# Kernel tuning notes

Measured on AMD Instinct MI355X. Metric: run time of the kernel, lower is better.

The kernel has to match this reference:

```python
import jax, jax.numpy as jnp
import numpy as np

E = 800000   # num edges
C = 64       # in_channels == out_channels
H = 4        # heads
D = C // H   # head_dim
N = 50000    # num_nodes


def setup_inputs() -> dict:
    key = jax.random.key(0)
    ks = jax.random.split(key, 10)
    s = 1.0 / np.sqrt(C)
    inp = {
        "query": jax.random.normal(ks[0], (E, C), jnp.float32),
        "key": jax.random.normal(ks[1], (E, C), jnp.float32),
        "value": jax.random.normal(ks[2], (E, C), jnp.float32),
        "Wq": jax.random.normal(ks[3], (C, C), jnp.float32) * s,
        "bq": jax.random.normal(ks[4], (C,), jnp.float32) * s,
        "Wk": jax.random.normal(ks[5], (C, C), jnp.float32) * s,
        "bk": jax.random.normal(ks[6], (C,), jnp.float32) * s,
        "Wv": jax.random.normal(ks[7], (C, C), jnp.float32) * s,
        "bv": jax.random.normal(ks[8], (C,), jnp.float32) * s,
        "index": jnp.sort(jax.random.randint(ks[9], (E,), 0, N, jnp.int32)),
        "num_nodes": N,
    }
    return inp


def reference(query, key, value, Wq, bq, Wk, bk, Wv, bv, index, num_nodes):
    # per-edge linear projections (groups=1 Linear)
    q = (query @ Wq + bq).reshape(E, H, D)
    k = (key @ Wk + bk).reshape(E, H, D)
    v = (value @ Wv + bv).reshape(E, H, D)

    # per-edge per-head scalar attention score
    score = jnp.einsum("ehd,ehd->eh", q, k) / jnp.sqrt(jnp.float32(D))  # [E, H]

    # restricted softmax over edges grouped by destination node (margin=0)
    smax = jax.ops.segment_max(score, index, num_segments=num_nodes)  # [N, H]
    smax = jnp.maximum(smax, 0.0)  # clamp(min=0); also fixes -inf on empty segments
    ex = jnp.exp(score - smax[index])                                  # [E, H]
    denom = jax.ops.segment_sum(ex, index, num_segments=num_nodes)    # [N, H]
    denom = denom + jnp.exp(-smax)                                     # margin - src_max with margin=0
    attn = ex / denom[index]                                           # [E, H]

    # weighted values (score is 1x1 per edge/head so this is a scale)
    out = attn[:, :, None] * v                                         # [E, H, D]
    return out.reshape(E, C)
```

## Files before the change

### kernel.cpp

```cpp
#include <hip/hip_runtime.h>
#include <hip/hip_bf16.h>
#include <math.h>

#define E_N 800000
#define C_N 64
#define H_N 4
#define D_N 16
#define NODES 50000

typedef __bf16 bf16x8 __attribute__((ext_vector_type(8)));
typedef float f32x4 __attribute__((ext_vector_type(4)));

__device__ __forceinline__ unsigned short f2bf_rne(float f) {
    unsigned int u = __float_as_uint(f);
    u += 0x7fffu + ((u >> 16) & 1u);
    return (unsigned short)(u >> 16);
}

union BfPack { bf16x8 v; unsigned short s[8]; };

__device__ __forceinline__ bf16x8 load_row_bf16(const float* __restrict__ p) {
    const float4* p4 = (const float4*)p;
    float4 a = p4[0], b = p4[1];
    BfPack u;
    u.s[0] = f2bf_rne(a.x); u.s[1] = f2bf_rne(a.y);
    u.s[2] = f2bf_rne(a.z); u.s[3] = f2bf_rne(a.w);
    u.s[4] = f2bf_rne(b.x); u.s[5] = f2bf_rne(b.y);
    u.s[6] = f2bf_rne(b.z); u.s[7] = f2bf_rne(b.w);
    return u.v;
}

__global__ void wt_kernel(const float* __restrict__ Wq,
                          const float* __restrict__ Wk,
                          const float* __restrict__ Wv,
                          unsigned short* __restrict__ wt) {
    int t = threadIdx.x;
    for (int w = 0; w < 3; ++w) {
        const float* W = (w == 0) ? Wq : (w == 1) ? Wk : Wv;
        for (int i = t; i < 4096; i += 256) {
            int o = i >> 6, c = i & 63;
            wt[w * 4096 + i] = f2bf_rne(W[c * 64 + o]);
        }
    }
}

__global__ __launch_bounds__(256) void score_kernel(
    const float* __restrict__ query, const float* __restrict__ key,
    const float* __restrict__ bq, const float* __restrict__ bk,
    const int* __restrict__ index,
    const unsigned short* __restrict__ wt,
    float* __restrict__ score, int* __restrict__ smax) {
    int lane = threadIdx.x & 63;
    int wid  = threadIdx.x >> 6;
    int e0   = blockIdx.x * 64 + wid * 16;
    int m    = lane & 15, quad = lane >> 4;

    const float* qrow = query + (size_t)(e0 + m) * 64 + quad * 8;
    const float* krow = key   + (size_t)(e0 + m) * 64 + quad * 8;
    bf16x8 aq0 = load_row_bf16(qrow);
    bf16x8 aq1 = load_row_bf16(qrow + 32);
    bf16x8 ak0 = load_row_bf16(krow);
    bf16x8 ak1 = load_row_bf16(krow + 32);

    const bf16x8* wq8 = (const bf16x8*)(wt);
    const bf16x8* wk8 = (const bf16x8*)(wt + 4096);

    for (int h = 0; h < H_N; ++h) {
        int bi0 = (h * 16 + m) * 8 + quad;
        int bi1 = bi0 + 4;
        f32x4 cq = {0.f, 0.f, 0.f, 0.f}, ck = {0.f, 0.f, 0.f, 0.f};
        cq = __builtin_amdgcn_mfma_f32_16x16x32_bf16(aq0, wq8[bi0], cq, 0, 0, 0);
        cq = __builtin_amdgcn_mfma_f32_16x16x32_bf16(aq1, wq8[bi1], cq, 0, 0, 0);
        ck = __builtin_amdgcn_mfma_f32_16x16x32_bf16(ak0, wk8[bi0], ck, 0, 0, 0);
        ck = __builtin_amdgcn_mfma_f32_16x16x32_bf16(ak1, wk8[bi1], ck, 0, 0, 0);
        float bqv = bq[h * 16 + m], bkv = bk[h * 16 + m];
        float p[4];
        #pragma unroll
        for (int r = 0; r < 4; ++r) p[r] = (cq[r] + bqv) * (ck[r] + bkv);
        #pragma unroll
        for (int r = 0; r < 4; ++r) {
            p[r] += __shfl_xor(p[r], 1, 64);
            p[r] += __shfl_xor(p[r], 2, 64);
            p[r] += __shfl_xor(p[r], 4, 64);
            p[r] += __shfl_xor(p[r], 8, 64);
        }
        if (m == 0) {
            #pragma unroll
            for (int r = 0; r < 4; ++r) {
                int e = e0 + quad * 4 + r;
                float s = p[r] * 0.25f;
                score[e * 4 + h] = s;
                if (s > 0.f) {
                    int n = index[e];
                    atomicMax(smax + n * 4 + h, __float_as_int(s));
                }
            }
        }
    }
}

__global__ void denom_init_kernel(const int* __restrict__ smax,
                                  float* __restrict__ denom) {
    int i = blockIdx.x * 256 + threadIdx.x;
    if (i < NODES * H_N) denom[i] = __expf(-__int_as_float(smax[i]));
}

__global__ __launch_bounds__(256) void expsum_kernel(
    const float* __restrict__ score, const int* __restrict__ index,
    const int* __restrict__ smax, float* __restrict__ denom) {
    int t = blockIdx.x * 256 + threadIdx.x;
    int e = t >> 2, h = t & 3;
    int n = index[e];
    float sm = __int_as_float(smax[n * 4 + h]);
    float ex = __expf(score[t] - sm);
    atomicAdd(denom + n * 4 + h, ex);
}

__global__ __launch_bounds__(256) void out_kernel(
    const float* __restrict__ value, const float* __restrict__ bv,
    const int* __restrict__ index, const unsigned short* __restrict__ wt,
    const float* __restrict__ score, const int* __restrict__ smax_i,
    const float* __restrict__ denom, float* __restrict__ out) {
    int lane = threadIdx.x & 63;
    int wid  = threadIdx.x >> 6;
    int e0   = blockIdx.x * 64 + wid * 16;
    int m    = lane & 15, quad = lane >> 4;

    int ee = e0 + (lane >> 2), hh = lane & 3;
    int n  = index[ee];
    float sm = __int_as_float(smax_i[n * 4 + hh]);
    float attn = __expf(score[ee * 4 + hh] - sm) / denom[n * 4 + hh];

    const float* vrow = value + (size_t)(e0 + m) * 64 + quad * 8;
    bf16x8 av0 = load_row_bf16(vrow);
    bf16x8 av1 = load_row_bf16(vrow + 32);
    const bf16x8* wv8 = (const bf16x8*)(wt + 8192);

    for (int h = 0; h < H_N; ++h) {
        int bi0 = (h * 16 + m) * 8 + quad;
        f32x4 cv = {0.f, 0.f, 0.f, 0.f};
        cv = __builtin_amdgcn_mfma_f32_16x16x32_bf16(av0, wv8[bi0], cv, 0, 0, 0);
        cv = __builtin_amdgcn_mfma_f32_16x16x32_bf16(av1, wv8[bi0 + 4], cv, 0, 0, 0);
        float bvv = bv[h * 16 + m];
        #pragma unroll
        for (int r = 0; r < 4; ++r) {
            int row = quad * 4 + r;
            float a = __shfl(attn, (row << 2) | h, 64);
            out[(size_t)(e0 + row) * 64 + h * 16 + m] = (cv[r] + bvv) * a;
        }
    }
}

extern "C" void kernel_launch(void* const* d_in, const int* in_sizes, int n_in,
                              void* d_out, int out_size, void* d_ws, size_t ws_size,
                              hipStream_t stream) {
    const float* query = (const float*)d_in[0];
    const float* key   = (const float*)d_in[1];
    const float* value = (const float*)d_in[2];
    const float* Wq    = (const float*)d_in[3];
    const float* bq    = (const float*)d_in[4];
    const float* Wk    = (const float*)d_in[5];
    const float* bk    = (const float*)d_in[6];
    const float* Wv    = (const float*)d_in[7];
    const float* bv    = (const float*)d_in[8];
    const int*   index = (const int*)d_in[9];

    char* ws = (char*)d_ws;
    unsigned short* wt = (unsigned short*)ws;
    float* score = (float*)(ws + 32768);
    int*   smax  = (int*)(ws + 32768 + (size_t)E_N * 16);
    float* denom = (float*)(ws + 32768 + (size_t)E_N * 16 + (size_t)NODES * 16);

    hipMemsetAsync(smax, 0, (size_t)NODES * 16, stream);
    wt_kernel<<<1, 256, 0, stream>>>(Wq, Wk, Wv, wt);
    score_kernel<<<E_N / 64, 256, 0, stream>>>(query, key, bq, bk, index, wt,
                                               score, smax);
    denom_init_kernel<<<(NODES * H_N + 255) / 256, 256, 0, stream>>>(smax, denom);
    expsum_kernel<<<(E_N * H_N) / 256, 256, 0, stream>>>(score, index, smax, denom);
    out_kernel<<<E_N / 64, 256, 0, stream>>>(value, bv, index, wt, score, smax,
                                             denom, (float*)d_out);
}
```

Measured before the change: 740.5 us.

## Pre-reduce segment max/sum within warps before atomics and precompute reciprocal denominators

Score and expsum kernels now do a segmented shuffle scan over the 16 edges per wave (using the sorted index) so only segment-tail lanes issue atomicMax/atomicAdd, cutting atomic traffic by the average in-wave run length. A finalize kernel folds the exp(-smax) term into the denominator and stores (smax, 1/denom) pairs, so out_kernel does one float2 load and a multiply instead of two loads and a divide. Score stores become coalesced one-per-lane rather than masked writes from m==0 lanes. It adds an extra index load per lane and one more small kernel launch.

```diff
diff --git a/kernel.cpp b/kernel.cpp
--- a/kernel.cpp
+++ b/kernel.cpp
@@ -65,6 +65,12 @@
     const bf16x8* wq8 = (const bf16x8*)(wt);
     const bf16x8* wk8 = (const bf16x8*)(wt + 4096);
 
+    int erel = lane >> 2;
+    int hl   = lane & 3;
+    int rw   = erel & 3;
+    float s_mine = 0.f;
+
+    #pragma unroll
     for (int h = 0; h < H_N; ++h) {
         int bi0 = (h * 16 + m) * 8 + quad;
         int bi1 = bi0 + 4;
@@ -84,58 +90,80 @@
             p[r] += __shfl_xor(p[r], 4, 64);
             p[r] += __shfl_xor(p[r], 8, 64);
         }
-        if (m == 0) {
-            #pragma unroll
-            for (int r = 0; r < 4; ++r) {
-                int e = e0 + quad * 4 + r;
-                float s = p[r] * 0.25f;
-                score[e * 4 + h] = s;
-                if (s > 0.f) {
-                    int n = index[e];
-                    atomicMax(smax + n * 4 + h, __float_as_int(s));
-                }
-            }
-        }
-    }
-}
-
-__global__ void denom_init_kernel(const int* __restrict__ smax,
-                                  float* __restrict__ denom) {
-    int i = blockIdx.x * 256 + threadIdx.x;
-    if (i < NODES * H_N) denom[i] = __expf(-__int_as_float(smax[i]));
+        float pw = (rw == 0) ? p[0] : (rw == 1) ? p[1] : (rw == 2) ? p[2] : p[3];
+        if (h == hl) s_mine = pw * 0.25f;
+    }
+
+    score[(size_t)e0 * 4 + lane] = s_mine;
+
+    int e = e0 + erel;
+    int n = index[e];
+    float s = s_mine;
+    #pragma unroll
+    for (int d = 4; d <= 32; d <<= 1) {
+        float up = __shfl_up(s, d, 64);
+        int  nup = __shfl_up(n, d, 64);
+        if (lane >= d && nup == n) s = fmaxf(s, up);
+    }
+    bool tail = (erel == 15) || (index[e + 1] != n);
+    if (tail && s > 0.f)
+        atomicMax(smax + n * 4 + hl, __float_as_int(s));
 }
 
 __global__ __launch_bounds__(256) void expsum_kernel(
     const float* __restrict__ score, const int* __restrict__ index,
     const int* __restrict__ smax, float* __restrict__ denom) {
-    int t = blockIdx.x * 256 + threadIdx.x;
-    int e = t >> 2, h = t & 3;
+    int lane = threadIdx.x & 63;
+    int wid  = threadIdx.x >> 6;
+    int e0   = blockIdx.x * 64 + wid * 16;
+    int erel = lane >> 2, h = lane & 3;
+    int e = e0 + erel;
     int n = index[e];
     float sm = __int_as_float(smax[n * 4 + h]);
-    float ex = __expf(score[t] - sm);
-    atomicAdd(denom + n * 4 + h, ex);
+    float s = __expf(score[(size_t)e0 * 4 + lane] - sm);
+    #pragma unroll
+    for (int d = 4; d <= 32; d <<= 1) {
+        float up = __shfl_up(s, d, 64);
+        int  nup = __shfl_up(n, d, 64);
+        if (lane >= d && nup == n) s += up;
+    }
+    bool tail = (erel == 15) || (index[e + 1] != n);
+    if (tail)
+        atomicAdd(denom + n * 4 + h, s);
+}
+
+__global__ void finalize_kernel(const int* __restrict__ smax,
+                                const float* __restrict__ denom,
+                                float2* __restrict__ nd) {
+    int i = blockIdx.x * 256 + threadIdx.x;
+    if (i < NODES * H_N) {
+        float sm = __int_as_float(smax[i]);
+        float d  = denom[i] + __expf(-sm);
+        nd[i] = make_float2(sm, 1.f / d);
+    }
 }
 
 __global__ __launch_bounds__(256) void out_kernel(
     const float* __restrict__ value, const float* __restrict__ bv,
     const int* __restrict__ index, const unsigned short* __restrict__ wt,
-    const float* __restrict__ score, const int* __restrict__ smax_i,
-    const float* __restrict__ denom, float* __restrict__ out) {
+    const float* __restrict__ score, const float2* __restrict__ nd,
+    float* __restrict__ out) {
     int lane = threadIdx.x & 63;
     int wid  = threadIdx.x >> 6;
     int e0   = blockIdx.x * 64 + wid * 16;
     int m    = lane & 15, quad = lane >> 4;
 
-    int ee = e0 + (lane >> 2), hh = lane & 3;
-    int n  = index[ee];
-    float sm = __int_as_float(smax_i[n * 4 + hh]);
-    float attn = __expf(score[ee * 4 + hh] - sm) / denom[n * 4 + hh];
+    int erel = lane >> 2, hl = lane & 3;
+    int n  = index[e0 + erel];
+    float2 t = nd[n * 4 + hl];
+    float attn = __expf(score[(size_t)e0 * 4 + lane] - t.x) * t.y;
 
     const float* vrow = value + (size_t)(e0 + m) * 64 + quad * 8;
     bf16x8 av0 = load_row_bf16(vrow);
     bf16x8 av1 = load_row_bf16(vrow + 32);
     const bf16x8* wv8 = (const bf16x8*)(wt + 8192);
 
+    #pragma unroll
     for (int h = 0; h < H_N; ++h) {
         int bi0 = (h * 16 + m) * 8 + quad;
         f32x4 cv = {0.f, 0.f, 0.f, 0.f};
@@ -168,15 +196,17 @@
     char* ws = (char*)d_ws;
     unsigned short* wt = (unsigned short*)ws;
     float* score = (float*)(ws + 32768);
-    int*   smax  = (int*)(ws + 32768 + (size_t)E_N * 16);
-    float* denom = (float*)(ws + 32768 + (size_t)E_N * 16 + (size_t)NODES * 16);
-
-    hipMemsetAsync(smax, 0, (size_t)NODES * 16, stream);
+    char*  p2    = ws + 32768 + (size_t)E_N * 16;
+    int*   smax  = (int*)p2;
+    float* denom = (float*)(p2 + (size_t)NODES * 16);
+    float2* nd   = (float2*)(p2 + 2 * (size_t)NODES * 16);
+
+    hipMemsetAsync(smax, 0, 2 * (size_t)NODES * 16, stream);
     wt_kernel<<<1, 256, 0, stream>>>(Wq, Wk, Wv, wt);
     score_kernel<<<E_N / 64, 256, 0, stream>>>(query, key, bq, bk, index, wt,
                                                score, smax);
-    denom_init_kernel<<<(NODES * H_N + 255) / 256, 256, 0, stream>>>(smax, denom);
-    expsum_kernel<<<(E_N * H_N) / 256, 256, 0, stream>>>(score, index, smax, denom);
-    out_kernel<<<E_N / 64, 256, 0, stream>>>(value, bv, index, wt, score, smax,
-                                             denom, (float*)d_out);
-}
+    expsum_kernel<<<E_N / 64, 256, 0, stream>>>(score, index, smax, denom);
+    finalize_kernel<<<(NODES * H_N + 255) / 256, 256, 0, stream>>>(smax, denom, nd);
+    out_kernel<<<E_N / 64, 256, 0, stream>>>(value, bv, index, wt, score, nd,
+                                             (float*)d_out);
+}
```

Result: faster. 669.9 us (-9.5%).
